# Performance work log

Measured on AMD Instinct MI355X. Metric: run time of the kernel, lower is better.

## Reference

```python
import jax, jax.numpy as jnp
import numpy as np

B, T, E, H = 8, 2048, 1024, 64

def setup_inputs() -> dict:
    key = jax.random.key(0)
    ks = jax.random.split(key, 7)
    s = 1.0 / np.sqrt(E)
    return {
        "x": jax.random.normal(ks[0], (B, T, E), dtype=jnp.float32),
        "Wk": jax.random.normal(ks[1], (E, H), dtype=jnp.float32) * s,
        "bk": jax.random.normal(ks[2], (H,), dtype=jnp.float32) * 0.01,
        "Wq": jax.random.normal(ks[3], (E, H), dtype=jnp.float32) * s,
        "bq": jax.random.normal(ks[4], (H,), dtype=jnp.float32) * 0.01,
        "Wv": jax.random.normal(ks[5], (E, H), dtype=jnp.float32) * s,
        "bv": jax.random.normal(ks[6], (H,), dtype=jnp.float32) * 0.01,
    }

def reference(x, Wk, bk, Wq, bq, Wv, bv):
    # q,k,v: [B, T, H]
    k = x @ Wk + bk
    q = x @ Wq + bq
    v = x @ Wv + bv
    scale = jnp.asarray(H, x.dtype) ** -0.5
    scores = jnp.einsum('bth,bsh->bts', q, k) * scale  # [B, T, T]
    T_ = x.shape[1]
    causal = jnp.tril(jnp.ones((T_, T_), dtype=bool))
    scores = jnp.where(causal, scores, jnp.asarray(-jnp.inf, x.dtype))
    attn = jax.nn.softmax(scores, axis=-1)  # dropout p=0.0 -> identity
    return jnp.einsum('bts,bsh->bth', attn, v)
```

## Files before the change

kernel.cpp:

```cpp
#include <hip/hip_runtime.h>
#include <hip/hip_bf16.h>
#include <math.h>

#define BB 8
#define TT 2048
#define EE 1024
#define HH 64
#define QSCALE 0.18033688011112042f

typedef __attribute__((ext_vector_type(8))) short short8;
typedef __attribute__((ext_vector_type(4))) float f32x4;
typedef __attribute__((ext_vector_type(16))) float f32x16;
typedef __attribute__((ext_vector_type(4))) unsigned short us4;

__device__ inline unsigned short f2bf(float f) {
  union { __hip_bfloat16 h; unsigned short u; } cv;
  cv.h = __float2bfloat16(f);
  return cv.u;
}

__global__ __launch_bounds__(256) void prep_w(
    const float* __restrict__ Wk, const float* __restrict__ Wq,
    const float* __restrict__ Wv, unsigned short* __restrict__ Wf) {
  const int idx = blockIdx.x * 256 + threadIdx.x;
  const int lane = idx & 63, ks = (idx >> 6) & 31, t = idx >> 11;
  const int q = lane & 15, g = lane >> 4;
  const int m = t >> 2, h = (t & 3) * 16 + q;
  const float* W = (m == 0) ? Wk : (m == 1) ? Wq : Wv;
  const float sc = (m == 1) ? QSCALE : 1.f;
  const int e0 = ks * 32 + g * 8;
  unsigned short v[8];
  #pragma unroll
  for (int j = 0; j < 8; ++j) v[j] = f2bf(W[(e0 + j) * 64 + h] * sc);
  *(short8*)&Wf[(size_t)idx * 8] = *(short8*)v;
}

__global__ __launch_bounds__(256) void qkv_proj(
    const float* __restrict__ x,
    const float* __restrict__ bk, const float* __restrict__ bq,
    const float* __restrict__ bv, const unsigned short* __restrict__ Wf,
    unsigned short* __restrict__ kf, unsigned short* __restrict__ qf,
    unsigned short* __restrict__ vf) {
  __shared__ alignas(16) unsigned short xs[2][32][264];

  const int tid = threadIdx.x;
  const long row0 = (long)blockIdx.x * 32;
  const int w = tid >> 6, lane = tid & 63;
  const int q = lane & 15, g = lane >> 4;

  const float4* xg = (const float4*)&x[row0 * EE];

  #pragma unroll
  for (int i = 0; i < 8; ++i) {
    const int flat = i * 256 + tid;
    const int rr = flat >> 6, c4 = flat & 63;
    const float4 xv = xg[rr * 256 + c4];
    us4 pk = {f2bf(xv.x), f2bf(xv.y), f2bf(xv.z), f2bf(xv.w)};
    *(us4*)&xs[0][rr][c4 * 4] = pk;
  }
  __syncthreads();

  const f32x4 z = {0.f, 0.f, 0.f, 0.f};
  f32x4 acc00 = z, acc01 = z, acc02 = z;
  f32x4 acc10 = z, acc11 = z, acc12 = z;
  const unsigned short* wf0 = &Wf[(size_t)(3 * w) * 16384 + (size_t)lane * 8];

  float4 st[8];
  #pragma unroll
  for (int cc = 0; cc < 4; ++cc) {
    if (cc < 3) {
      #pragma unroll
      for (int i = 0; i < 8; ++i) {
        const int flat = i * 256 + tid;
        const int rr = flat >> 6, c4 = flat & 63;
        st[i] = xg[rr * 256 + (cc + 1) * 64 + c4];
      }
    }
    #pragma unroll
    for (int ksl = 0; ksl < 8; ++ksl) {
      const short8 a0 = *(const short8*)&xs[cc & 1][q][ksl * 32 + g * 8];
      const short8 a1 = *(const short8*)&xs[cc & 1][16 + q][ksl * 32 + g * 8];
      const int ks = cc * 8 + ksl;
      const short8 b0 = *(const short8*)&wf0[ks * 512];
      const short8 b1 = *(const short8*)&wf0[16384 + ks * 512];
      const short8 b2 = *(const short8*)&wf0[32768 + ks * 512];
      acc00 = __builtin_amdgcn_mfma_f32_16x16x32_bf16(a0, b0, acc00, 0, 0, 0);
      acc10 = __builtin_amdgcn_mfma_f32_16x16x32_bf16(a1, b0, acc10, 0, 0, 0);
      acc01 = __builtin_amdgcn_mfma_f32_16x16x32_bf16(a0, b1, acc01, 0, 0, 0);
      acc11 = __builtin_amdgcn_mfma_f32_16x16x32_bf16(a1, b1, acc11, 0, 0, 0);
      acc02 = __builtin_amdgcn_mfma_f32_16x16x32_bf16(a0, b2, acc02, 0, 0, 0);
      acc12 = __builtin_amdgcn_mfma_f32_16x16x32_bf16(a1, b2, acc12, 0, 0, 0);
    }
    if (cc < 3) {
      #pragma unroll
      for (int i = 0; i < 8; ++i) {
        const int flat = i * 256 + tid;
        const int rr = flat >> 6, c4 = flat & 63;
        us4 pk = {f2bf(st[i].x), f2bf(st[i].y), f2bf(st[i].z), f2bf(st[i].w)};
        *(us4*)&xs[(cc + 1) & 1][rr][c4 * 4] = pk;
      }
    }
    __syncthreads();
  }

  const long bidx = row0 >> 11;
  const int tl0 = (int)(row0 & 2047);
  #pragma unroll
  for (int i = 0; i < 3; ++i) {
    const int tgl = 3 * w + i;
    const int mm = tgl >> 2, hb = tgl & 3;
    const int h = hb * 16 + q;
    const float bias = (mm == 0) ? bk[h] : (mm == 1) ? bq[h] * QSCALE : bv[h];
    #pragma unroll
    for (int stp = 0; stp < 2; ++stp) {
      const f32x4 a = (stp == 0) ? ((i == 0) ? acc00 : (i == 1) ? acc01 : acc02)
                                 : ((i == 0) ? acc10 : (i == 1) ? acc11 : acc12);
      #pragma unroll
      for (int r = 0; r < 4; ++r) {
        const int tl = tl0 + stp * 16 + 4 * g + r;
        const unsigned short ov = f2bf(a[r] + bias);
        if (mm == 2) {
          const int lane32v = ((hb & 1) * 16 + q) + 32 * ((tl >> 3) & 1);
          const size_t vidx = (size_t)bidx * 131072 + (size_t)(tl >> 5) * 2048 +
                              (size_t)(hb >> 1) * 1024 +
                              (size_t)((tl >> 4) & 1) * 512 +
                              (size_t)lane32v * 8 + (size_t)(tl & 7);
          vf[vidx] = ov;
        } else {
          const int lane32 = (tl & 31) + 32 * ((q >> 3) & 1);
          const size_t kqidx = (size_t)bidx * 131072 + (size_t)(tl >> 5) * 2048 +
                               (size_t)hb * 512 + (size_t)lane32 * 8 +
                               (size_t)(q & 7);
          if (mm == 0) kf[kqidx] = ov; else qf[kqidx] = ov;
        }
      }
    }
  }
}

#define BODY(KC, KN, tt, PREF) do {                                          \
    const unsigned short* vp_ = vfb + (size_t)(tt) * 2048;                   \
    const short8 V00 = *(const short8*)&vp_[0];                              \
    const short8 V10 = *(const short8*)&vp_[1024];                           \
    if (PREF) {                                                              \
      const unsigned short* kp_ = kfb + (size_t)((tt) + stride) * 2048;      \
      KN[0] = *(const short8*)&kp_[0];                                       \
      KN[1] = *(const short8*)&kp_[512];                                     \
      KN[2] = *(const short8*)&kp_[1024];                                    \
      KN[3] = *(const short8*)&kp_[1536];                                    \
    }                                                                        \
    f32x16 S;                                                                \
    _Pragma("unroll")                                                        \
    for (int r = 0; r < 16; ++r) S[r] = 0.f;                                 \
    __builtin_amdgcn_s_setprio(1);                                           \
    S = __builtin_amdgcn_mfma_f32_32x32x16_bf16(KC[0], Qf0, S, 0, 0, 0);     \
    S = __builtin_amdgcn_mfma_f32_32x32x16_bf16(KC[1], Qf1, S, 0, 0, 0);     \
    S = __builtin_amdgcn_mfma_f32_32x32x16_bf16(KC[2], Qf2, S, 0, 0, 0);     \
    S = __builtin_amdgcn_mfma_f32_32x32x16_bf16(KC[3], Qf3, S, 0, 0, 0);     \
    __builtin_amdgcn_s_setprio(0);                                           \
    const int k0_ = (tt) * 32;                                               \
    if (k0_ + 31 > q0) {                                                     \
      _Pragma("unroll")                                                      \
      for (int r = 0; r < 16; ++r) {                                         \
        const int key = (r & 3) + 8 * (r >> 2) + 4 * hf;                     \
        if (k0_ + key > qg) S[r] = -INFINITY;                                \
      }                                                                      \
    }                                                                        \
    float pmax = S[0];                                                       \
    _Pragma("unroll")                                                        \
    for (int r = 1; r < 16; ++r) pmax = fmaxf(pmax, S[r]);                   \
    if (!__all(pmax <= m + 8.0f)) {                                          \
      const float pm2 = fmaxf(pmax, __shfl_xor(pmax, 32));                   \
      const float nm = fmaxf(m, pm2);                                        \
      const float rs = __builtin_amdgcn_exp2f(m - nm);                       \
      l *= rs;                                                               \
      _Pragma("unroll")                                                      \
      for (int r = 0; r < 16; ++r) { O0[r] *= rs; O1[r] *= rs; }             \
      m = nm;                                                                \
    }                                                                        \
    float ps = 0.f;                                                          \
    _Pragma("unroll")                                                        \
    for (int r = 0; r < 16; ++r) {                                           \
      S[r] = __builtin_amdgcn_exp2f(S[r] - m); ps += S[r];                   \
    }                                                                        \
    l += ps;                                                                 \
    unsigned wa0, wa1, wa2, wa3, wb0, wb1, wb2, wb3;                         \
    asm("v_cvt_pk_bf16_f32 %0, %1, %2" : "=v"(wa0) : "v"(S[0]), "v"(S[1])); \
    asm("v_cvt_pk_bf16_f32 %0, %1, %2" : "=v"(wb0) : "v"(S[2]), "v"(S[3])); \
    asm("v_cvt_pk_bf16_f32 %0, %1, %2" : "=v"(wa1) : "v"(S[4]), "v"(S[5])); \
    asm("v_cvt_pk_bf16_f32 %0, %1, %2" : "=v"(wb1) : "v"(S[6]), "v"(S[7])); \
    asm("v_cvt_pk_bf16_f32 %0, %1, %2" : "=v"(wa2) : "v"(S[8]), "v"(S[9])); \
    asm("v_cvt_pk_bf16_f32 %0, %1, %2" : "=v"(wb2) : "v"(S[10]), "v"(S[11]));\
    asm("v_cvt_pk_bf16_f32 %0, %1, %2" : "=v"(wa3) : "v"(S[12]), "v"(S[13]));\
    asm("v_cvt_pk_bf16_f32 %0, %1, %2" : "=v"(wb3) : "v"(S[14]), "v"(S[15]));\
    {                                  \
      const unsigned sA = hf ? wa1 : wa0, sB = hf ? wb1 : wb0;               \
      const unsigned tA = hf ? wa0 : wa1, tB = hf ? wb0 : wb1;               \
      const unsigned xA = __shfl_xor((int)tA, 32);                           \
      const unsigned xB = __shfl_xor((int)tB, 32);                           \
      union { unsigned u[4]; short8 s; } pf_;                                \
      pf_.u[0] = hf ? xA : sA; pf_.u[1] = hf ? xB : sB;                      \
      pf_.u[2] = hf ? sA : xA; pf_.u[3] = hf ? sB : xB;                      \
      __builtin_amdgcn_s_setprio(1);                                         \
      O0 = __builtin_amdgcn_mfma_f32_32x32x16_bf16(V00, pf_.s, O0, 0, 0, 0); \
      O1 = __builtin_amdgcn_mfma_f32_32x32x16_bf16(V10, pf_.s, O1, 0, 0, 0); \
      __builtin_amdgcn_s_setprio(0);                                         \
    }                                                                        \
    {                                                  \
      const short8 V01 = *(const short8*)&vp_[512];                          \
      const short8 V11 = *(const short8*)&vp_[1536];                         \
      const unsigned sA = hf ? wa3 : wa2, sB = hf ? wb3 : wb2;               \
      const unsigned tA = hf ? wa2 : wa3, tB = hf ? wb2 : wb3;               \
      const unsigned xA = __shfl_xor((int)tA, 32);                           \
      const unsigned xB = __shfl_xor((int)tB, 32);                           \
      union { unsigned u[4]; short8 s; } pf_;                                \
      pf_.u[0] = hf ? xA : sA; pf_.u[1] = hf ? xB : sB;                      \
      pf_.u[2] = hf ? sA : xA; pf_.u[3] = hf ? sB : xB;                      \
      __builtin_amdgcn_s_setprio(1);                                         \
      O0 = __builtin_amdgcn_mfma_f32_32x32x16_bf16(V01, pf_.s, O0, 0, 0, 0); \
      O1 = __builtin_amdgcn_mfma_f32_32x32x16_bf16(V11, pf_.s, O1, 0, 0, 0); \
      __builtin_amdgcn_s_setprio(0);                                         \
    }                                                                        \
  } while (0)

__global__ __launch_bounds__(512, 4) void attn_fwd(
    const unsigned short* __restrict__ qf, const unsigned short* __restrict__ kf,
    const unsigned short* __restrict__ vf, float* __restrict__ out) {
  __shared__ float accS[8][32][65];
  __shared__ float mlS[8][2][32];

  const int tid = threadIdx.x;
  const int w = tid >> 6, lane = tid & 63;
  const int q = lane & 31, hf = lane >> 5;

  const int b = blockIdx.x & 7;
  const int p = blockIdx.x >> 3;
  const int s1 = 63 - p;
  const int nt0 = p + 1, nt1 = 64 - p;
  int k = (8 * nt0 + 32) / 65;
  if (k < 1) k = 1;
  if (k > 7) k = 7;

  const bool onS0 = (w < k);
  const int s = onS0 ? p : s1;
  const int nt = onS0 ? nt0 : nt1;
  const int stride = onS0 ? k : (8 - k);
  int t = onS0 ? w : (w - k);

  const int q0 = s * 32;
  const int qg = q0 + q;

  const unsigned short* kfb = kf + (size_t)b * 131072 + (size_t)lane * 8;
  const unsigned short* vfb = vf + (size_t)b * 131072 + (size_t)lane * 8;
  const unsigned short* qfb = qf + (size_t)b * 131072 + (size_t)s * 2048 +
                              (size_t)lane * 8;
  const short8 Qf0 = *(const short8*)&qfb[0];
  const short8 Qf1 = *(const short8*)&qfb[512];
  const short8 Qf2 = *(const short8*)&qfb[1024];
  const short8 Qf3 = *(const short8*)&qfb[1536];

  float m = -3.0e38f, l = 0.f;
  f32x16 O0, O1;
  #pragma unroll
  for (int r = 0; r < 16; ++r) { O0[r] = 0.f; O1[r] = 0.f; }

  {
    short8 A[4], B[4];
    const unsigned short* kp0 = kfb + (size_t)t * 2048;
    A[0] = *(const short8*)&kp0[0];
    A[1] = *(const short8*)&kp0[512];
    A[2] = *(const short8*)&kp0[1024];
    A[3] = *(const short8*)&kp0[1536];
    for (;;) {
      bool pf = (t + stride) < nt;
      BODY(A, B, t, pf);
      if (!pf) break;
      t += stride;
      pf = (t + stride) < nt;
      BODY(B, A, t, pf);
      if (!pf) break;
      t += stride;
    }
  }

  const float lq = l + __shfl_xor(l, 32);
  #pragma unroll
  for (int r = 0; r < 16; ++r) {
    const int hh0 = (r & 3) + 8 * (r >> 2) + 4 * hf;
    accS[w][q][hh0] = O0[r];
    accS[w][q][hh0 + 32] = O1[r];
  }
  if (hf == 0) { mlS[w][0][q] = m; mlS[w][1][q] = lq; }
  __syncthreads();

  const int half_t = tid >> 8;
  const int sm = half_t ? s1 : p;
  const int lo = half_t ? k : 0, hi2 = half_t ? 8 : k;
  const int hh = tid & 63;
  const int qb0 = (tid >> 6) & 3;
  const long obase = ((long)b * TT + (long)sm * 32) * 64;
  #pragma unroll
  for (int kk = 0; kk < 8; ++kk) {
    const int qv = qb0 + 4 * kk;
    float M = -INFINITY;
    for (int i = lo; i < hi2; ++i) M = fmaxf(M, mlS[i][0][qv]);
    float L = 0.f, acc = 0.f;
    for (int i = lo; i < hi2; ++i) {
      const float fi = __builtin_amdgcn_exp2f(mlS[i][0][qv] - M);
      L += fi * mlS[i][1][qv];
      acc += fi * accS[i][qv][hh];
    }
    out[obase + (long)qv * 64 + hh] = acc / L;
  }
}

extern "C" void kernel_launch(void* const* d_in, const int* in_sizes, int n_in,
                              void* d_out, int out_size, void* d_ws, size_t ws_size,
                              hipStream_t stream) {
  const float* x  = (const float*)d_in[0];
  const float* Wk = (const float*)d_in[1];
  const float* bk = (const float*)d_in[2];
  const float* Wq = (const float*)d_in[3];
  const float* bq = (const float*)d_in[4];
  const float* Wv = (const float*)d_in[5];
  const float* bv = (const float*)d_in[6];
  float* out = (float*)d_out;

  unsigned short* qfb = (unsigned short*)d_ws;
  unsigned short* kfb = qfb + (size_t)1048576;
  unsigned short* vfb = kfb + (size_t)1048576;
  unsigned short* Wf  = vfb + (size_t)1048576;

  prep_w<<<dim3(96), 256, 0, stream>>>(Wk, Wq, Wv, Wf);
  qkv_proj<<<dim3(512), 256, 0, stream>>>(x, bk, bq, bv, Wf, kfb, qfb, vfb);
  attn_fwd<<<dim3(256), 512, 0, stream>>>(qfb, kfb, vfb, out);
}
```

Measured before the change: 51.89 us.

## Stage QKV output tile in LDS for coalesced stores; double attention waves per block

```diff
diff --git a/kernel.cpp b/kernel.cpp
--- a/kernel.cpp
+++ b/kernel.cpp
@@ -103,8 +103,7 @@
     __syncthreads();
   }
 
-  const long bidx = row0 >> 11;
-  const int tl0 = (int)(row0 & 2047);
+  unsigned short* img = (unsigned short*)xs;
   #pragma unroll
   for (int i = 0; i < 3; ++i) {
     const int tgl = 3 * w + i;
@@ -117,25 +116,26 @@
                                  : ((i == 0) ? acc10 : (i == 1) ? acc11 : acc12);
       #pragma unroll
       for (int r = 0; r < 4; ++r) {
-        const int tl = tl0 + stp * 16 + 4 * g + r;
+        const int tl5 = stp * 16 + 4 * g + r;
         const unsigned short ov = f2bf(a[r] + bias);
         if (mm == 2) {
-          const int lane32v = ((hb & 1) * 16 + q) + 32 * ((tl >> 3) & 1);
-          const size_t vidx = (size_t)bidx * 131072 + (size_t)(tl >> 5) * 2048 +
-                              (size_t)(hb >> 1) * 1024 +
-                              (size_t)((tl >> 4) & 1) * 512 +
-                              (size_t)lane32v * 8 + (size_t)(tl & 7);
-          vf[vidx] = ov;
+          const int lane32v = ((hb & 1) * 16 + q) + 32 * ((tl5 >> 3) & 1);
+          img[4096 + (hb >> 1) * 1024 + ((tl5 >> 4) & 1) * 512 +
+              lane32v * 8 + (tl5 & 7)] = ov;
         } else {
-          const int lane32 = (tl & 31) + 32 * ((q >> 3) & 1);
-          const size_t kqidx = (size_t)bidx * 131072 + (size_t)(tl >> 5) * 2048 +
-                               (size_t)hb * 512 + (size_t)lane32 * 8 +
-                               (size_t)(q & 7);
-          if (mm == 0) kf[kqidx] = ov; else qf[kqidx] = ov;
+          const int lane32 = tl5 + 32 * ((q >> 3) & 1);
+          img[mm * 2048 + hb * 512 + lane32 * 8 + (q & 7)] = ov;
         }
       }
     }
   }
+  __syncthreads();
+  const size_t obase = (size_t)(row0 >> 11) * 131072 +
+                       (size_t)((row0 & 2047) >> 5) * 2048;
+  const int o = tid * 8;
+  *(short8*)&kf[obase + o] = *(const short8*)&img[o];
+  *(short8*)&qf[obase + o] = *(const short8*)&img[2048 + o];
+  *(short8*)&vf[obase + o] = *(const short8*)&img[4096 + o];
 }
 
 #define BODY(KC, KN, tt, PREF) do {                                          \
@@ -223,11 +223,11 @@
     }                                                                        \
   } while (0)
 
-__global__ __launch_bounds__(512, 4) void attn_fwd(
+__global__ __launch_bounds__(1024, 4) void attn_fwd(
     const unsigned short* __restrict__ qf, const unsigned short* __restrict__ kf,
     const unsigned short* __restrict__ vf, float* __restrict__ out) {
-  __shared__ float accS[8][32][65];
-  __shared__ float mlS[8][2][32];
+  __shared__ float accS[16][32][65];
+  __shared__ float mlS[16][2][32];
 
   const int tid = threadIdx.x;
   const int w = tid >> 6, lane = tid & 63;
@@ -237,14 +237,14 @@
   const int p = blockIdx.x >> 3;
   const int s1 = 63 - p;
   const int nt0 = p + 1, nt1 = 64 - p;
-  int k = (8 * nt0 + 32) / 65;
+  int k = (16 * nt0 + 32) / 65;
   if (k < 1) k = 1;
-  if (k > 7) k = 7;
+  if (k > 15) k = 15;
 
   const bool onS0 = (w < k);
   const int s = onS0 ? p : s1;
   const int nt = onS0 ? nt0 : nt1;
-  const int stride = onS0 ? k : (8 - k);
+  const int stride = onS0 ? k : (16 - k);
   int t = onS0 ? w : (w - k);
 
   const int q0 = s * 32;
@@ -293,15 +293,16 @@
   if (hf == 0) { mlS[w][0][q] = m; mlS[w][1][q] = lq; }
   __syncthreads();
 
-  const int half_t = tid >> 8;
+  const int half_t = tid >> 9;
   const int sm = half_t ? s1 : p;
-  const int lo = half_t ? k : 0, hi2 = half_t ? 8 : k;
-  const int hh = tid & 63;
-  const int qb0 = (tid >> 6) & 3;
+  const int lo = half_t ? k : 0, hi2 = half_t ? 16 : k;
+  const int idx = tid & 511;
+  const int hh = idx & 63;
+  const int qb0 = idx >> 6;
   const long obase = ((long)b * TT + (long)sm * 32) * 64;
   #pragma unroll
-  for (int kk = 0; kk < 8; ++kk) {
-    const int qv = qb0 + 4 * kk;
+  for (int kk = 0; kk < 4; ++kk) {
+    const int qv = qb0 + 8 * kk;
     float M = -INFINITY;
     for (int i = lo; i < hi2; ++i) M = fmaxf(M, mlS[i][0][qv]);
     float L = 0.f, acc = 0.f;
@@ -333,5 +334,5 @@
 
   prep_w<<<dim3(96), 256, 0, stream>>>(Wk, Wq, Wv, Wf);
   qkv_proj<<<dim3(512), 256, 0, stream>>>(x, bk, bq, bv, Wf, kfb, qfb, vfb);
-  attn_fwd<<<dim3(256), 512, 0, stream>>>(qfb, kfb, vfb, out);
-}
+  attn_fwd<<<dim3(256), 1024, 0, stream>>>(qfb, kfb, vfb, out);
+}
```

After: 52.35 us. Within noise of the previous version (+0.9%).
